# Kernel optimization log

Hardware: AMD Instinct MI355X
Metric: run time of the kernel (lower is better)

Reference implementation:

```python
import jax, jax.numpy as jnp
import numpy as np

N = 8192
F_IN = 512
F_OUT = 256
NEG_SLOPE = 0.01  # F.leaky_relu default
MASK_VAL = -1000000000000000.0


def setup_inputs() -> dict:
    key = jax.random.key(0)
    k1, k2, k3, k4 = jax.random.split(key, 4)
    stdv = 1.0 / np.sqrt(F_OUT)
    x = jax.random.normal(k1, (N, F_IN), dtype=jnp.float32)
    weight = jax.random.uniform(k2, (F_IN, F_OUT), dtype=jnp.float32, minval=-stdv, maxval=stdv)
    att_vec = jax.random.normal(k3, (2 * F_OUT, 1), dtype=jnp.float32) * 0.05
    adj = jax.random.randint(k4, (N, N), 0, 2, dtype=jnp.int32)
    return {"x": x, "weight": weight, "att_vec": att_vec, "adj": adj}


def _pair_indices(n):
    # Reproduces the (buggy-but-faithful) torch.cat(dim=0).view(n,-1,2f) indexing:
    # element (i,j,:f)  = out[idx(2m)], element (i,j,f:) = out[idx(2m+1)], m = i*n+j
    # idx(r) = r // n if r < n*n else (r - n*n) % n
    nn_ = n * n
    m = jnp.arange(nn_, dtype=jnp.int32)
    r0 = 2 * m
    r1 = r0 + 1
    idx1 = jnp.where(r0 < nn_, r0 // n, (r0 - nn_) % n)
    idx2 = jnp.where(r1 < nn_, r1 // n, (r1 - nn_) % n)
    return idx1, idx2


def reference(x, weight, att_vec, adj):
    n = x.shape[0]
    f = weight.shape[1]
    # dropout p=0.0 -> identity
    out = x @ weight                      # (n, f)
    a1 = att_vec[:f, 0]                   # (f,)
    a2 = att_vec[f:, 0]                   # (f,)
    s1 = out @ a1                         # (n,)
    s2 = out @ a2                         # (n,)
    idx1, idx2 = _pair_indices(n)
    scores = (s1[idx1] + s2[idx2]).reshape(n, n)
    scores = jax.nn.leaky_relu(scores, NEG_SLOPE)
    scores = jnp.where(adj > 0, scores, MASK_VAL)
    attn = jax.nn.softmax(scores, axis=1)  # F.softmax default dim=1 for 2D
    return jax.nn.sigmoid(attn @ out)      # (n, f)
```

## Files before the change

kernel.cpp:

```cpp
#include <hip/hip_runtime.h>

using u32 = unsigned int;
using u16 = unsigned short;

typedef __attribute__((ext_vector_type(8)))  __bf16 bf16x8;
typedef __attribute__((ext_vector_type(16))) float  f32x16;
typedef __attribute__((ext_vector_type(4)))  float  f32x4;
typedef __attribute__((ext_vector_type(4)))  int    i32x4;

__device__ __forceinline__ u32 f2bf(float f){
  u32 u = __float_as_uint(f);
  return (u + 0x7FFFu + ((u >> 16) & 1u)) >> 16;
}
__device__ __forceinline__ u32 pack2bf(float lo, float hi){
  return f2bf(lo) | (f2bf(hi) << 16);
}
__device__ __forceinline__ float bfu2f(u32 us){ return __uint_as_float(us << 16); }
__device__ __forceinline__ float lrelu(float x){ return x > 0.f ? x : 0.01f * x; }

__global__ void k0_wt(const float* __restrict__ w, u16* __restrict__ wT){
  int u = blockIdx.x * 256 + threadIdx.x;
  int k = u >> 8, n = u & 255;
  wT[(size_t)n * 512 + k] = (u16)f2bf(w[(size_t)k * 256 + n]);
}

__global__ __launch_bounds__(512, 2) void k1_gemm(const float* __restrict__ x,
    const u16* __restrict__ wT, const float* __restrict__ av, u16* __restrict__ outF,
    float* __restrict__ v0, float* __restrict__ v1, u16* __restrict__ pbf){
  __shared__ float tb[8][32][36];
  __shared__ float afl[512];
  __shared__ float sred[2][32][17];
  __shared__ float srw[2][32];
  const int i0 = blockIdx.x * 32;
  const int tid = threadIdx.x;
  const int lane = tid & 63, wv = tid >> 6;
  const int r = lane & 31, h = lane >> 5;
  const float* xp = x + (size_t)(i0 + r) * 512 + h * 8;
  const u16*   bp = wT + (size_t)(wv * 32 + r) * 512 + h * 8;
  f32x16 acc = {};
  for (int s = 0; s < 32; ++s){
    f32x4 a0 = *(const f32x4*)xp;
    f32x4 a1 = *(const f32x4*)(xp + 4);
    i32x4 pk = { (int)pack2bf(a0[0], a0[1]), (int)pack2bf(a0[2], a0[3]),
                 (int)pack2bf(a1[0], a1[1]), (int)pack2bf(a1[2], a1[3]) };
    bf16x8 af = __builtin_bit_cast(bf16x8, pk);
    bf16x8 bf = *(const bf16x8*)bp;
    acc = __builtin_amdgcn_mfma_f32_32x32x16_bf16(af, bf, acc, 0, 0, 0);
    xp += 16; bp += 16;
  }
  #pragma unroll
  for (int re = 0; re < 16; ++re){
    int rr = (re & 3) + 8 * (re >> 2) + 4 * h;
    tb[wv][r][rr] = acc[re];
  }
  afl[tid] = av[tid];
  __syncthreads();
  {
    const int n2 = lane >> 1, ic = (lane & 1) * 16;
    const float* tp = &tb[wv][n2][ic];
    i32x4 w0 = { (int)pack2bf(tp[0],tp[1]),   (int)pack2bf(tp[2],tp[3]),
                 (int)pack2bf(tp[4],tp[5]),   (int)pack2bf(tp[6],tp[7]) };
    i32x4 w1 = { (int)pack2bf(tp[8],tp[9]),   (int)pack2bf(tp[10],tp[11]),
                 (int)pack2bf(tp[12],tp[13]), (int)pack2bf(tp[14],tp[15]) };
    const int n = wv * 32 + n2;
    const int k16 = (i0 + ic) >> 4;
    u16* op = outF + ((size_t)k16 * 256 + n) * 16;
    *(i32x4*)op = w0;
    *((i32x4*)op + 1) = w1;
  }
  const int row = tid & 31, g = tid >> 5;
  const int w8 = g >> 1, fh = (g & 1) * 16;
  float a1c = 0.f, a2c = 0.f;
  #pragma unroll
  for (int f = 0; f < 16; ++f){
    float tv = tb[w8][fh + f][row];
    a1c = fmaf(tv, afl[w8 * 32 + fh + f], a1c);
    a2c = fmaf(tv, afl[256 + w8 * 32 + fh + f], a2c);
  }
  sred[0][row][g] = a1c; sred[1][row][g] = a2c;
  __syncthreads();
  if (tid < 64){
    int which = tid >> 5, r2 = tid & 31;
    float s = 0.f;
    #pragma unroll
    for (int g2 = 0; g2 < 16; ++g2) s += sred[which][r2][g2];
    srw[which][r2] = s;
  }
  __syncthreads();
  if (tid < 16){
    int k = (i0 >> 1) + tid;
    float sa  = srw[0][2*tid],   sb  = srw[1][2*tid];
    float sa1 = srw[0][2*tid+1], sb1 = srw[1][2*tid+1];
    v0[k] = lrelu(sa + sb);
    v1[k] = lrelu(sa1 + sb1);
    float w = lrelu(sa + sb1);
    pbf[k] = (u16)f2bf(__expf(w));
  }
}

__global__ __launch_bounds__(512, 2) void k3_main(const int* __restrict__ adj,
    const u16* __restrict__ outF, const u16* __restrict__ pbf,
    float* __restrict__ P, float* __restrict__ pd){
  __shared__ u16 Ab[2][4096];
  __shared__ u32 pl32[1024];
  __shared__ float dred[64][9];
  const int bid = blockIdx.x;
  const int xcd = bid & 7, slot = bid >> 3;
  const bool top = xcd < 4;
  const int c = top ? xcd : xcd - 4;
  const int gt = (top ? 0 : 64) + slot;
  const int i0 = gt * 64;
  const int kbase = c * 2048;
  const int pb = gt * 4 + c;
  const int tid = threadIdx.x, lane = tid & 63, wv = tid >> 6;
  const int r = lane & 31, h = lane >> 5, fb = wv * 32;
  const int srow = tid >> 3, sc = tid & 7;
  const int h8 = h * 8;
  const int* aq0 = adj + (size_t)(i0 + srow) * 8192 + kbase + sc * 8;
  const u16* bq0 = outF + ((size_t)(kbase >> 4) * 256 + fb + r) * 16 + h8;
  u16* const wp0 = &Ab[0][0] + sc * 512 + ((srow ^ sc) * 8);
  const u32* const pq0 = pl32 + sc * 4;

  if (top){
    pl32[tid] = 0x3F803F80u; pl32[tid + 512] = 0x3F803F80u;
  } else {
    const u32* ps = (const u32*)pbf + (c & 1) * 1024;
    pl32[tid] = ps[tid]; pl32[tid + 512] = ps[tid + 512];
  }
  __syncthreads();

  i32x4 aA0, aA1, aB0, aB1;
  bf16x8 BA[4], BB[4];
  f32x16 acc0 = {}, acc1 = {};
  float d = 0.f;

#define ADJ_A(S_) { const int* ap_ = aq0 + (S_) * 64; \
  aA0 = __builtin_nontemporal_load((const i32x4*)ap_); \
  aA1 = __builtin_nontemporal_load((const i32x4*)(ap_ + 4)); \
  asm volatile("" ::: "memory"); }
#define ADJ_B(S_) { const int* ap_ = aq0 + (S_) * 64; \
  aB0 = __builtin_nontemporal_load((const i32x4*)ap_); \
  aB1 = __builtin_nontemporal_load((const i32x4*)(ap_ + 4)); \
  asm volatile("" ::: "memory"); }

#define B_ISS(B_,S_) { const u16* bb_ = bq0 + (size_t)(S_) * 16384; \
  _Pragma("unroll") for (int ks = 0; ks < 4; ++ks) \
    B_[ks] = *(const bf16x8*)(bb_ + ks * 4096); \
  asm volatile("" ::: "memory"); }

#define MFMA8(B_,BUF_) { const u16* rb_ = &Ab[BUF_][0]; \
  __builtin_amdgcn_s_setprio(1); \
  _Pragma("unroll") for (int ks = 0; ks < 4; ++ks){ \
    const int cc_ = ks * 2 + h; \
    bf16x8 a0_ = *(const bf16x8*)(rb_ + cc_ * 512 + ((r ^ cc_) * 8)); \
    bf16x8 a1_ = *(const bf16x8*)(rb_ + cc_ * 512 + (((32 + r) ^ cc_) * 8)); \
    acc0 = __builtin_amdgcn_mfma_f32_32x32x16_bf16(a0_, B_[ks], acc0, 0, 0, 0); \
    acc1 = __builtin_amdgcn_mfma_f32_32x32x16_bf16(a1_, B_[ks], acc1, 0, 0, 0); } \
  __builtin_amdgcn_s_setprio(0); }

#define PACKW(A0_,A1_,BUF_,S_) { \
  i32x4 pv_ = *(const i32x4*)(pq0 + (S_) * 32); \
  u32 w0_ = ((((u32)(-A0_[0])) & 0xFFFFu) | (((u32)(-A0_[1])) << 16)) & (u32)pv_[0]; \
  u32 w1_ = ((((u32)(-A0_[2])) & 0xFFFFu) | (((u32)(-A0_[3])) << 16)) & (u32)pv_[1]; \
  u32 w2_ = ((((u32)(-A1_[0])) & 0xFFFFu) | (((u32)(-A1_[1])) << 16)) & (u32)pv_[2]; \
  u32 w3_ = ((((u32)(-A1_[2])) & 0xFFFFu) | (((u32)(-A1_[3])) << 16)) & (u32)pv_[3]; \
  d += __uint_as_float(w0_ << 16) + __uint_as_float(w0_ & 0xFFFF0000u); \
  d += __uint_as_float(w1_ << 16) + __uint_as_float(w1_ & 0xFFFF0000u); \
  d += __uint_as_float(w2_ << 16) + __uint_as_float(w2_ & 0xFFFF0000u); \
  d += __uint_as_float(w3_ << 16) + __uint_as_float(w3_ & 0xFFFF0000u); \
  i32x4 wv_ = { (int)w0_, (int)w1_, (int)w2_, (int)w3_ }; \
  *(i32x4*)(wp0 + (BUF_) * 4096) = wv_; }

#define KBAR() { asm volatile("s_waitcnt lgkmcnt(0)" ::: "memory"); \
  __builtin_amdgcn_s_barrier(); asm volatile("" ::: "memory"); }

  ADJ_A(0);
  B_ISS(BA, 0);
  ADJ_B(1);
  PACKW(aA0, aA1, 0, 0);
  KBAR();
  #pragma unroll 1
  for (int s = 0; s < 28; s += 2){
    B_ISS(BB, s + 1);  ADJ_A(s + 2);  MFMA8(BA, 0);  PACKW(aB0, aB1, 1, s + 1);  KBAR();
    B_ISS(BA, s + 2);  ADJ_B(s + 3);  MFMA8(BB, 1);  PACKW(aA0, aA1, 0, s + 2);  KBAR();
  }
  B_ISS(BB, 29);  ADJ_A(30);  MFMA8(BA, 0);  PACKW(aB0, aB1, 1, 29);  KBAR();
  B_ISS(BA, 30);  ADJ_B(31);  MFMA8(BB, 1);  PACKW(aA0, aA1, 0, 30);  KBAR();
  B_ISS(BB, 31);              MFMA8(BA, 0);  PACKW(aB0, aB1, 1, 31);  KBAR();
  MFMA8(BB, 1);

#undef ADJ_A
#undef ADJ_B
#undef B_ISS
#undef MFMA8
#undef PACKW
#undef KBAR

  dred[srow][sc] = d;
  __syncthreads();
  if (tid < 64){
    float s = 0.f;
    #pragma unroll
    for (int q = 0; q < 8; ++q) s += dred[tid][q];
    pd[(size_t)pb * 64 + tid] = s;
  }
  float* Pb = P + (size_t)pb * 16384 + fb + r;
  #pragma unroll
  for (int e = 0; e < 16; ++e){
    int rr = (e & 3) + 8 * (e >> 2) + 4 * h;
    __builtin_nontemporal_store(acc0[e], Pb + (size_t)rr * 256);
    __builtin_nontemporal_store(acc1[e], Pb + (size_t)(rr + 32) * 256);
  }
}

__global__ void k4_final(const float* __restrict__ P, const float* __restrict__ pd,
    const float* __restrict__ v0, const float* __restrict__ v1, float* __restrict__ out){
  const int i = blockIdx.x, n = threadIdx.x;
  const int tile = i >> 6, rloc = i & 63;
  const size_t base = ((size_t)tile * 4 * 64 + rloc) * 256 + n;
  float P0 = __builtin_nontemporal_load(P + base);
  float P1 = __builtin_nontemporal_load(P + base + 16384);
  float P2 = __builtin_nontemporal_load(P + base + 32768);
  float P3 = __builtin_nontemporal_load(P + base + 49152);
  const float* pdp = pd + (size_t)tile * 256 + rloc;
  float d0 = pdp[0], d1 = pdp[64], d2 = pdp[128], d3 = pdp[192];
  float val;
  if (i < 4096){
    float va = v0[i], vb = v1[i];
    float m = fmaxf(va, vb);
    float e0 = __expf(va - m), e1 = __expf(vb - m);
    val = (e0 * (P0 + P1) + e1 * (P2 + P3)) / (e0 * (d0 + d1) + e1 * (d2 + d3));
  } else {
    val = (P0 + P1 + P2 + P3) / (d0 + d1 + d2 + d3);
  }
  out[(size_t)i * 256 + n] = 1.0f / (1.0f + __expf(-val));
}

extern "C" void kernel_launch(void* const* d_in, const int* in_sizes, int n_in,
                              void* d_out, int out_size, void* d_ws, size_t ws_size,
                              hipStream_t stream)
{
  const float* x      = (const float*)d_in[0];
  const float* weight = (const float*)d_in[1];
  const float* av     = (const float*)d_in[2];
  const int*   adj    = (const int*)d_in[3];
  float* out = (float*)d_out;
  char* ws = (char*)d_ws;
  float* P     = (float*)(ws + 0);
  float* pd    = (float*)(ws + 33554432);
  u16*   outF  = (u16*)  (ws + 33685504);
  u16*   wT    = (u16*)  (ws + 37879808);
  u16*   pbf   = (u16*)  (ws + 38141952);
  float* v0    = (float*)(ws + 38150144);
  float* v1    = (float*)(ws + 38166528);

  k0_wt    <<<512, 256, 0, stream>>>(weight, wT);
  k1_gemm  <<<256, 512, 0, stream>>>(x, wT, av, outF, v0, v1, pbf);
  k3_main  <<<512, 512, 0, stream>>>(adj, outF, pbf, P, pd);
  k4_final <<<8192, 256, 0, stream>>>(P, pd, v0, v1, out);
}
```

Measured before the change: 129.4 us.

## Halve row tile to 32 rows, double grid, restructure adj loading and packing

The main attention-aggregation kernel now handles 32 query rows per block instead of 64, with 1024 blocks. Each block uses a single 32x32 MFMA accumulator and processes 128-wide k steps with 8 MFMAs per stage. Adjacency rows are now loaded one row per wave with contiguous lane addressing, and the packed bf16 mask is written into a new unswizzled LDS layout by half the lanes per stage. The final kernel's indexing is updated to match the new partial-result layout. This gives more parallelism and better adj coalescing, but each block reuses its outF B-tile across fewer rows, so B traffic per row doubles.

After: 116.8 us. -9.7%, faster.

```diff
diff --git a/kernel.cpp b/kernel.cpp
--- a/kernel.cpp
+++ b/kernel.cpp
@@ -103,23 +103,20 @@
     float* __restrict__ P, float* __restrict__ pd){
   __shared__ u16 Ab[2][4096];
   __shared__ u32 pl32[1024];
-  __shared__ float dred[64][9];
+  __shared__ float dred[32][66];
   const int bid = blockIdx.x;
   const int xcd = bid & 7, slot = bid >> 3;
-  const bool top = xcd < 4;
-  const int c = top ? xcd : xcd - 4;
-  const int gt = (top ? 0 : 64) + slot;
-  const int i0 = gt * 64;
+  const int c = xcd >> 1;
+  const int tile = (xcd & 1) * 128 + slot;
+  const bool top = tile < 128;
+  const int i0 = tile * 32;
   const int kbase = c * 2048;
-  const int pb = gt * 4 + c;
-  const int tid = threadIdx.x, lane = tid & 63, wv = tid >> 6;
-  const int r = lane & 31, h = lane >> 5, fb = wv * 32;
-  const int srow = tid >> 3, sc = tid & 7;
-  const int h8 = h * 8;
-  const int* aq0 = adj + (size_t)(i0 + srow) * 8192 + kbase + sc * 8;
-  const u16* bq0 = outF + ((size_t)(kbase >> 4) * 256 + fb + r) * 16 + h8;
-  u16* const wp0 = &Ab[0][0] + sc * 512 + ((srow ^ sc) * 8);
-  const u32* const pq0 = pl32 + sc * 4;
+  const int pb = tile * 4 + c;
+  const int tid = threadIdx.x, l = tid & 63, w = tid >> 6;
+  const int r = l & 31, h = l >> 5;
+  const int fb = w * 32;
+  const int* aq0 = adj + (size_t)(i0 + w) * 8192 + kbase + l * 4;
+  const u16* bq0 = outF + ((size_t)(kbase >> 4) * 256 + fb + r) * 16 + h * 8;
 
   if (top){
     pl32[tid] = 0x3F803F80u; pl32[tid + 512] = 0x3F803F80u;
@@ -129,101 +126,101 @@
   }
   __syncthreads();
 
-  i32x4 aA0, aA1, aB0, aB1;
-  bf16x8 BA[4], BB[4];
-  f32x16 acc0 = {}, acc1 = {};
-  float d = 0.f;
-
-#define ADJ_A(S_) { const int* ap_ = aq0 + (S_) * 64; \
-  aA0 = __builtin_nontemporal_load((const i32x4*)ap_); \
-  aA1 = __builtin_nontemporal_load((const i32x4*)(ap_ + 4)); \
+  i32x4 ar[4];
+  bf16x8 BA[8], BB[8];
+  f32x16 acc = {};
+  float d4[4] = {0.f, 0.f, 0.f, 0.f};
+
+#define ADJ_ISS(PP_) { \
+  _Pragma("unroll") for (int q = 0; q < 4; ++q) \
+    ar[q] = *(const i32x4*)(aq0 + (size_t)q * 65536 + (PP_) * 256); \
   asm volatile("" ::: "memory"); }
-#define ADJ_B(S_) { const int* ap_ = aq0 + (S_) * 64; \
-  aB0 = __builtin_nontemporal_load((const i32x4*)ap_); \
-  aB1 = __builtin_nontemporal_load((const i32x4*)(ap_ + 4)); \
+
+#define B_ISS(B_,T_) { const u16* bb_ = bq0 + (size_t)(T_) * 32768; \
+  _Pragma("unroll") for (int j = 0; j < 8; ++j) \
+    B_[j] = *(const bf16x8*)(bb_ + j * 4096); \
   asm volatile("" ::: "memory"); }
 
-#define B_ISS(B_,S_) { const u16* bb_ = bq0 + (size_t)(S_) * 16384; \
-  _Pragma("unroll") for (int ks = 0; ks < 4; ++ks) \
-    B_[ks] = *(const bf16x8*)(bb_ + ks * 4096); \
-  asm volatile("" ::: "memory"); }
-
-#define MFMA8(B_,BUF_) { const u16* rb_ = &Ab[BUF_][0]; \
+#define MFMA8(B_,BUF_) { const u16* rb_ = &Ab[BUF_][0] + r * 16 + h * 8; \
   __builtin_amdgcn_s_setprio(1); \
-  _Pragma("unroll") for (int ks = 0; ks < 4; ++ks){ \
-    const int cc_ = ks * 2 + h; \
-    bf16x8 a0_ = *(const bf16x8*)(rb_ + cc_ * 512 + ((r ^ cc_) * 8)); \
-    bf16x8 a1_ = *(const bf16x8*)(rb_ + cc_ * 512 + (((32 + r) ^ cc_) * 8)); \
-    acc0 = __builtin_amdgcn_mfma_f32_32x32x16_bf16(a0_, B_[ks], acc0, 0, 0, 0); \
-    acc1 = __builtin_amdgcn_mfma_f32_32x32x16_bf16(a1_, B_[ks], acc1, 0, 0, 0); } \
+  _Pragma("unroll") for (int j = 0; j < 8; ++j){ \
+    bf16x8 a_ = *(const bf16x8*)(rb_ + j * 512); \
+    acc = __builtin_amdgcn_mfma_f32_32x32x16_bf16(a_, B_[j], acc, 0, 0, 0); } \
   __builtin_amdgcn_s_setprio(0); }
 
-#define PACKW(A0_,A1_,BUF_,S_) { \
-  i32x4 pv_ = *(const i32x4*)(pq0 + (S_) * 32); \
-  u32 w0_ = ((((u32)(-A0_[0])) & 0xFFFFu) | (((u32)(-A0_[1])) << 16)) & (u32)pv_[0]; \
-  u32 w1_ = ((((u32)(-A0_[2])) & 0xFFFFu) | (((u32)(-A0_[3])) << 16)) & (u32)pv_[1]; \
-  u32 w2_ = ((((u32)(-A1_[0])) & 0xFFFFu) | (((u32)(-A1_[1])) << 16)) & (u32)pv_[2]; \
-  u32 w3_ = ((((u32)(-A1_[2])) & 0xFFFFu) | (((u32)(-A1_[3])) << 16)) & (u32)pv_[3]; \
-  d += __uint_as_float(w0_ << 16) + __uint_as_float(w0_ & 0xFFFF0000u); \
-  d += __uint_as_float(w1_ << 16) + __uint_as_float(w1_ & 0xFFFF0000u); \
-  d += __uint_as_float(w2_ << 16) + __uint_as_float(w2_ & 0xFFFF0000u); \
-  d += __uint_as_float(w3_ << 16) + __uint_as_float(w3_ & 0xFFFF0000u); \
-  i32x4 wv_ = { (int)w0_, (int)w1_, (int)w2_, (int)w3_ }; \
-  *(i32x4*)(wp0 + (BUF_) * 4096) = wv_; }
+#define PACKW(H_,BUF_,PP_) { \
+  if ((l >> 5) == (H_)){ \
+    const int ks_ = (l & 31) >> 2; \
+    u32 pv0_ = pl32[(PP_) * 128 + l * 2]; \
+    u32 pv1_ = pl32[(PP_) * 128 + l * 2 + 1]; \
+    u16* wb_ = &Ab[BUF_][0] + ks_ * 512 + (l & 3) * 4; \
+    _Pragma("unroll") for (int q = 0; q < 4; ++q){ \
+      i32x4 a_ = ar[q]; \
+      u32 w0_ = ((((u32)(-a_[0])) & 0xFFFFu) | (((u32)(-a_[1])) << 16)) & pv0_; \
+      u32 w1_ = ((((u32)(-a_[2])) & 0xFFFFu) | (((u32)(-a_[3])) << 16)) & pv1_; \
+      d4[q] += __uint_as_float(w0_ << 16) + __uint_as_float(w0_ & 0xFFFF0000u) \
+             + __uint_as_float(w1_ << 16) + __uint_as_float(w1_ & 0xFFFF0000u); \
+      uint2 wv_; wv_.x = w0_; wv_.y = w1_; \
+      *(uint2*)(wb_ + (q * 8 + w) * 16) = wv_; } } }
 
 #define KBAR() { asm volatile("s_waitcnt lgkmcnt(0)" ::: "memory"); \
   __builtin_amdgcn_s_barrier(); asm volatile("" ::: "memory"); }
 
-  ADJ_A(0);
+  ADJ_ISS(0);
   B_ISS(BA, 0);
-  ADJ_B(1);
-  PACKW(aA0, aA1, 0, 0);
+  PACKW(0, 0, 0);
   KBAR();
   #pragma unroll 1
-  for (int s = 0; s < 28; s += 2){
-    B_ISS(BB, s + 1);  ADJ_A(s + 2);  MFMA8(BA, 0);  PACKW(aB0, aB1, 1, s + 1);  KBAR();
-    B_ISS(BA, s + 2);  ADJ_B(s + 3);  MFMA8(BB, 1);  PACKW(aA0, aA1, 0, s + 2);  KBAR();
-  }
-  B_ISS(BB, 29);  ADJ_A(30);  MFMA8(BA, 0);  PACKW(aB0, aB1, 1, 29);  KBAR();
-  B_ISS(BA, 30);  ADJ_B(31);  MFMA8(BB, 1);  PACKW(aA0, aA1, 0, 30);  KBAR();
-  B_ISS(BB, 31);              MFMA8(BA, 0);  PACKW(aB0, aB1, 1, 31);  KBAR();
+  for (int pp = 0; pp < 8; ++pp){
+    const int e = 2 * pp;
+    B_ISS(BB, e + 1);
+    MFMA8(BA, 0);
+    PACKW(1, 1, pp);
+    if (pp < 7) ADJ_ISS(pp + 1);
+    KBAR();
+    if (pp < 7){
+      B_ISS(BA, e + 2);
+      MFMA8(BB, 1);
+      PACKW(0, 0, pp + 1);
+      KBAR();
+    }
+  }
   MFMA8(BB, 1);
 
-#undef ADJ_A
-#undef ADJ_B
+#undef ADJ_ISS
 #undef B_ISS
 #undef MFMA8
 #undef PACKW
 #undef KBAR
 
-  dred[srow][sc] = d;
-  __syncthreads();
-  if (tid < 64){
+  #pragma unroll
+  for (int q = 0; q < 4; ++q) dred[q * 8 + w][l] = d4[q];
+  __syncthreads();
+  if (tid < 32){
     float s = 0.f;
     #pragma unroll
-    for (int q = 0; q < 8; ++q) s += dred[tid][q];
-    pd[(size_t)pb * 64 + tid] = s;
-  }
-  float* Pb = P + (size_t)pb * 16384 + fb + r;
-  #pragma unroll
-  for (int e = 0; e < 16; ++e){
-    int rr = (e & 3) + 8 * (e >> 2) + 4 * h;
-    __builtin_nontemporal_store(acc0[e], Pb + (size_t)rr * 256);
-    __builtin_nontemporal_store(acc1[e], Pb + (size_t)(rr + 32) * 256);
+    for (int j = 0; j < 64; ++j) s += dred[tid][j];
+    pd[(size_t)pb * 32 + tid] = s;
+  }
+  float* Pb = P + (size_t)pb * 8192 + fb + r;
+  #pragma unroll
+  for (int e2 = 0; e2 < 16; ++e2){
+    int rr = (e2 & 3) + 8 * (e2 >> 2) + 4 * h;
+    __builtin_nontemporal_store(acc[e2], Pb + (size_t)rr * 256);
   }
 }
 
 __global__ void k4_final(const float* __restrict__ P, const float* __restrict__ pd,
     const float* __restrict__ v0, const float* __restrict__ v1, float* __restrict__ out){
   const int i = blockIdx.x, n = threadIdx.x;
-  const int tile = i >> 6, rloc = i & 63;
-  const size_t base = ((size_t)tile * 4 * 64 + rloc) * 256 + n;
+  const int tile = i >> 5, rloc = i & 31;
+  const size_t base = (size_t)tile * 32768 + (size_t)rloc * 256 + n;
   float P0 = __builtin_nontemporal_load(P + base);
-  float P1 = __builtin_nontemporal_load(P + base + 16384);
-  float P2 = __builtin_nontemporal_load(P + base + 32768);
-  float P3 = __builtin_nontemporal_load(P + base + 49152);
-  const float* pdp = pd + (size_t)tile * 256 + rloc;
-  float d0 = pdp[0], d1 = pdp[64], d2 = pdp[128], d3 = pdp[192];
+  float P1 = __builtin_nontemporal_load(P + base + 8192);
+  float P2 = __builtin_nontemporal_load(P + base + 16384);
+  float P3 = __builtin_nontemporal_load(P + base + 24576);
+  const float* pdp = pd + (size_t)tile * 128 + rloc;
+  float d0 = pdp[0], d1 = pdp[32], d2 = pdp[64], d3 = pdp[96];
   float val;
   if (i < 4096){
     float va = v0[i], vb = v1[i];
@@ -256,6 +253,6 @@
 
   k0_wt    <<<512, 256, 0, stream>>>(weight, wT);
   k1_gemm  <<<256, 512, 0, stream>>>(x, wT, av, outF, v0, v1, pbf);
-  k3_main  <<<512, 512, 0, stream>>>(adj, outF, pbf, P, pd);
+  k3_main  <<<1024, 512, 0, stream>>>(adj, outF, pbf, P, pd);
   k4_final <<<8192, 256, 0, stream>>>(P, pd, v0, v1, out);
 }
```

## Restructure k3 main loop into larger K stages with row-per-wave adj loads

Applied to the files above, without the earlier changes.

Reorganizes the adjacency-times-features kernel so each stage stages a 256-wide K chunk (four sub-steps) in padded LDS instead of a 64-wide one, cutting barriers from 32 to 8 per block. Each wave now loads adj rows directly with lane-contiguous 16-byte loads, and the row denominators are reduced with wave shuffles instead of an LDS table. Block-to-tile mapping across XCDs is also changed. The larger LDS footprint (about 67KB) and more live registers may limit occupancy at the requested two blocks per CU. A dead overwritten expression was added in k4.

Result: faster. 111.2 us (-14.0%).

```diff
diff --git a/kernel.cpp b/kernel.cpp
--- a/kernel.cpp
+++ b/kernel.cpp
@@ -101,109 +101,120 @@
 __global__ __launch_bounds__(512, 2) void k3_main(const int* __restrict__ adj,
     const u16* __restrict__ outF, const u16* __restrict__ pbf,
     float* __restrict__ P, float* __restrict__ pd){
-  __shared__ u16 Ab[2][4096];
-  __shared__ u32 pl32[1024];
-  __shared__ float dred[64][9];
+  __shared__ u16 AbS[2][16768];
+  __shared__ u32 plS[1024];
+  __shared__ float dshS[64];
   const int bid = blockIdx.x;
   const int xcd = bid & 7, slot = bid >> 3;
-  const bool top = xcd < 4;
-  const int c = top ? xcd : xcd - 4;
-  const int gt = (top ? 0 : 64) + slot;
-  const int i0 = gt * 64;
+  const int half = xcd & 1, c = xcd >> 1;
+  const int tile = half * 64 + slot;
+  const bool top = half == 0;
+  const int i0 = tile * 64;
   const int kbase = c * 2048;
-  const int pb = gt * 4 + c;
-  const int tid = threadIdx.x, lane = tid & 63, wv = tid >> 6;
-  const int r = lane & 31, h = lane >> 5, fb = wv * 32;
-  const int srow = tid >> 3, sc = tid & 7;
-  const int h8 = h * 8;
-  const int* aq0 = adj + (size_t)(i0 + srow) * 8192 + kbase + sc * 8;
-  const u16* bq0 = outF + ((size_t)(kbase >> 4) * 256 + fb + r) * 16 + h8;
-  u16* const wp0 = &Ab[0][0] + sc * 512 + ((srow ^ sc) * 8);
-  const u32* const pq0 = pl32 + sc * 4;
+  const int pb = tile * 4 + c;
+  const int tid = threadIdx.x, l = tid & 63, w = tid >> 6;
+  const int r = l & 31, h = l >> 5, fb = w * 32;
+  const int* aq0 = adj + (size_t)(i0 + w) * 8192 + kbase + l * 4;
+  const u16* bq0 = outF + (size_t)c * 524288 + (fb + r) * 16 + h * 8;
+  const int sl_ = l >> 2, hp_ = (l >> 1) & 1, off_ = 4 * (l & 1);
+  u16* const wp0 = &AbS[0][0] + sl_ * 1048 + hp_ * 512 + off_;
+  const u16* const rp0 = &AbS[0][0] + h * 512 + r * 8;
 
   if (top){
-    pl32[tid] = 0x3F803F80u; pl32[tid + 512] = 0x3F803F80u;
+    plS[tid] = 0x3F803F80u; plS[tid + 512] = 0x3F803F80u;
   } else {
     const u32* ps = (const u32*)pbf + (c & 1) * 1024;
-    pl32[tid] = ps[tid]; pl32[tid + 512] = ps[tid + 512];
-  }
-  __syncthreads();
-
-  i32x4 aA0, aA1, aB0, aB1;
+    plS[tid] = ps[tid]; plS[tid + 512] = ps[tid + 512];
+  }
+  __syncthreads();
+
+  i32x4 arA[4], arB[4];
   bf16x8 BA[4], BB[4];
   f32x16 acc0 = {}, acc1 = {};
-  float d = 0.f;
-
-#define ADJ_A(S_) { const int* ap_ = aq0 + (S_) * 64; \
-  aA0 = __builtin_nontemporal_load((const i32x4*)ap_); \
-  aA1 = __builtin_nontemporal_load((const i32x4*)(ap_ + 4)); \
+  float dA[4] = {0.f,0.f,0.f,0.f}, dB[4] = {0.f,0.f,0.f,0.f};
+
+#define ADJ_SET(AR_,Q0_,T_) { \
+  _Pragma("unroll") for (int q_ = 0; q_ < 4; ++q_) \
+    AR_[q_] = *(const i32x4*)(aq0 + (size_t)((Q0_) + q_) * 65536 + (T_) * 256); \
   asm volatile("" ::: "memory"); }
-#define ADJ_B(S_) { const int* ap_ = aq0 + (S_) * 64; \
-  aB0 = __builtin_nontemporal_load((const i32x4*)ap_); \
-  aB1 = __builtin_nontemporal_load((const i32x4*)(ap_ + 4)); \
+
+#define B_ISS4(B_,G_) { const u16* bb_ = bq0 + (size_t)(G_) * 4096; \
+  B_[0] = *(const bf16x8*)bb_;          B_[1] = *(const bf16x8*)(bb_ + 4096); \
+  B_[2] = *(const bf16x8*)(bb_ + 8192); B_[3] = *(const bf16x8*)(bb_ + 12288); \
   asm volatile("" ::: "memory"); }
 
-#define B_ISS(B_,S_) { const u16* bb_ = bq0 + (size_t)(S_) * 16384; \
-  _Pragma("unroll") for (int ks = 0; ks < 4; ++ks) \
-    B_[ks] = *(const bf16x8*)(bb_ + ks * 4096); \
-  asm volatile("" ::: "memory"); }
-
-#define MFMA8(B_,BUF_) { const u16* rb_ = &Ab[BUF_][0]; \
+#define MFMA4(B_,BUF_,S0_) { \
+  const u16* rb_ = rp0 + (BUF_) * 16768 + (S0_) * 1048; \
   __builtin_amdgcn_s_setprio(1); \
-  _Pragma("unroll") for (int ks = 0; ks < 4; ++ks){ \
-    const int cc_ = ks * 2 + h; \
-    bf16x8 a0_ = *(const bf16x8*)(rb_ + cc_ * 512 + ((r ^ cc_) * 8)); \
-    bf16x8 a1_ = *(const bf16x8*)(rb_ + cc_ * 512 + (((32 + r) ^ cc_) * 8)); \
-    acc0 = __builtin_amdgcn_mfma_f32_32x32x16_bf16(a0_, B_[ks], acc0, 0, 0, 0); \
-    acc1 = __builtin_amdgcn_mfma_f32_32x32x16_bf16(a1_, B_[ks], acc1, 0, 0, 0); } \
+  _Pragma("unroll") for (int j_ = 0; j_ < 4; ++j_){ \
+    bf16x8 a0_ = *(const bf16x8*)(rb_ + j_ * 1048); \
+    bf16x8 a1_ = *(const bf16x8*)(rb_ + j_ * 1048 + 256); \
+    acc0 = __builtin_amdgcn_mfma_f32_32x32x16_bf16(a0_, B_[j_], acc0, 0, 0, 0); \
+    acc1 = __builtin_amdgcn_mfma_f32_32x32x16_bf16(a1_, B_[j_], acc1, 0, 0, 0); } \
   __builtin_amdgcn_s_setprio(0); }
 
-#define PACKW(A0_,A1_,BUF_,S_) { \
-  i32x4 pv_ = *(const i32x4*)(pq0 + (S_) * 32); \
-  u32 w0_ = ((((u32)(-A0_[0])) & 0xFFFFu) | (((u32)(-A0_[1])) << 16)) & (u32)pv_[0]; \
-  u32 w1_ = ((((u32)(-A0_[2])) & 0xFFFFu) | (((u32)(-A0_[3])) << 16)) & (u32)pv_[1]; \
-  u32 w2_ = ((((u32)(-A1_[0])) & 0xFFFFu) | (((u32)(-A1_[1])) << 16)) & (u32)pv_[2]; \
-  u32 w3_ = ((((u32)(-A1_[2])) & 0xFFFFu) | (((u32)(-A1_[3])) << 16)) & (u32)pv_[3]; \
-  d += __uint_as_float(w0_ << 16) + __uint_as_float(w0_ & 0xFFFF0000u); \
-  d += __uint_as_float(w1_ << 16) + __uint_as_float(w1_ & 0xFFFF0000u); \
-  d += __uint_as_float(w2_ << 16) + __uint_as_float(w2_ & 0xFFFF0000u); \
-  d += __uint_as_float(w3_ << 16) + __uint_as_float(w3_ & 0xFFFF0000u); \
-  i32x4 wv_ = { (int)w0_, (int)w1_, (int)w2_, (int)w3_ }; \
-  *(i32x4*)(wp0 + (BUF_) * 4096) = wv_; }
+#define PACK_SET(AR_,D_,RB_,T_,BUF_) { \
+  _Pragma("unroll") for (int q_ = 0; q_ < 4; ++q_){ \
+    const int row_ = (RB_) * 32 + q_ * 8 + w; \
+    i32x4 a_ = AR_[q_]; \
+    u32 p0_ = plS[((T_) & 7) * 128 + 2 * l]; \
+    u32 p1_ = plS[((T_) & 7) * 128 + 2 * l + 1]; \
+    u32 w0_ = ((((u32)(-a_[0])) & 0xFFFFu) | (((u32)(-a_[1])) << 16)) & p0_; \
+    u32 w1_ = ((((u32)(-a_[2])) & 0xFFFFu) | (((u32)(-a_[3])) << 16)) & p1_; \
+    D_[q_] += __uint_as_float(w0_ << 16) + __uint_as_float(w0_ & 0xFFFF0000u) \
+            + __uint_as_float(w1_ << 16) + __uint_as_float(w1_ & 0xFFFF0000u); \
+    uint2 wv_; wv_.x = w0_; wv_.y = w1_; \
+    *(uint2*)(wp0 + (BUF_) * 16768 + row_ * 8) = wv_; } }
 
 #define KBAR() { asm volatile("s_waitcnt lgkmcnt(0)" ::: "memory"); \
   __builtin_amdgcn_s_barrier(); asm volatile("" ::: "memory"); }
 
-  ADJ_A(0);
-  B_ISS(BA, 0);
-  ADJ_B(1);
-  PACKW(aA0, aA1, 0, 0);
+  ADJ_SET(arA, 0, 0);
+  ADJ_SET(arB, 4, 0);
+  B_ISS4(BA, 0);
+  PACK_SET(arA, dA, 0, 0, 0);
+  PACK_SET(arB, dB, 1, 0, 0);
   KBAR();
+
   #pragma unroll 1
-  for (int s = 0; s < 28; s += 2){
-    B_ISS(BB, s + 1);  ADJ_A(s + 2);  MFMA8(BA, 0);  PACKW(aB0, aB1, 1, s + 1);  KBAR();
-    B_ISS(BA, s + 2);  ADJ_B(s + 3);  MFMA8(BB, 1);  PACKW(aA0, aA1, 0, s + 2);  KBAR();
-  }
-  B_ISS(BB, 29);  ADJ_A(30);  MFMA8(BA, 0);  PACKW(aB0, aB1, 1, 29);  KBAR();
-  B_ISS(BA, 30);  ADJ_B(31);  MFMA8(BB, 1);  PACKW(aA0, aA1, 0, 30);  KBAR();
-  B_ISS(BB, 31);              MFMA8(BA, 0);  PACKW(aB0, aB1, 1, 31);  KBAR();
-  MFMA8(BB, 1);
-
-#undef ADJ_A
-#undef ADJ_B
-#undef B_ISS
-#undef MFMA8
-#undef PACKW
+  for (int t = 0; t < 8; ++t){
+    const int buf = t & 1;
+    const int g0 = t * 16;
+    B_ISS4(BB, g0 + 4);
+    if (t < 7) ADJ_SET(arA, 0, t + 1);
+    MFMA4(BA, buf, 0);
+    B_ISS4(BA, g0 + 8);
+    if (t < 7) ADJ_SET(arB, 4, t + 1);
+    MFMA4(BB, buf, 4);
+    B_ISS4(BB, g0 + 12);
+    MFMA4(BA, buf, 8);
+    if (t < 7){ B_ISS4(BA, g0 + 16); }
+    MFMA4(BB, buf, 12);
+    if (t < 7){
+      PACK_SET(arA, dA, 0, t + 1, buf ^ 1);
+      PACK_SET(arB, dB, 1, t + 1, buf ^ 1);
+      KBAR();
+    }
+  }
+
+#undef ADJ_SET
+#undef B_ISS4
+#undef MFMA4
+#undef PACK_SET
 #undef KBAR
 
-  dred[srow][sc] = d;
-  __syncthreads();
-  if (tid < 64){
-    float s = 0.f;
+  #pragma unroll
+  for (int q = 0; q < 4; ++q){
+    float vA = dA[q], vB = dB[q];
     #pragma unroll
-    for (int q = 0; q < 8; ++q) s += dred[tid][q];
-    pd[(size_t)pb * 64 + tid] = s;
-  }
+    for (int mk = 1; mk < 64; mk <<= 1){
+      vA += __shfl_xor(vA, mk);
+      vB += __shfl_xor(vB, mk);
+    }
+    if (l == 0){ dshS[q * 8 + w] = vA; dshS[32 + q * 8 + w] = vB; }
+  }
+  __syncthreads();
+  if (tid < 64) pd[(size_t)pb * 64 + tid] = dshS[tid];
   float* Pb = P + (size_t)pb * 16384 + fb + r;
   #pragma unroll
   for (int e = 0; e < 16; ++e){
@@ -229,6 +240,8 @@
     float va = v0[i], vb = v1[i];
     float m = fmaxf(va, vb);
     float e0 = __expf(va - m), e1 = __expf(vb - m);
+    val = (e0 * (P0 + P1 + P2 + P3) * 0.f + e0 * (P0 + P1 + P2 + P3)) /
+          (1.f);
     val = (e0 * (P0 + P1) + e1 * (P2 + P3)) / (e0 * (d0 + d1) + e1 * (d2 + d3));
   } else {
     val = (P0 + P1 + P2 + P3) / (d0 + d1 + d2 + d3);
```
